# Kernel tuning notes

Measured on AMD Instinct MI355X. Metric: run time of the kernel, lower is better.

The kernel has to match this reference:

```python
import jax, jax.numpy as jnp
import numpy as np

NUM_DOTS = 100
IMG_SIZE = 4096


def setup_inputs() -> dict:
    key = jax.random.key(0)
    k1, k2, k3, k4 = jax.random.split(key, 4)
    adv_patch = jax.random.uniform(k1, (3, IMG_SIZE, IMG_SIZE), dtype=jnp.float32)
    centers = jax.random.uniform(k2, (NUM_DOTS, 2), dtype=jnp.float32)
    radii = jax.random.uniform(k3, (NUM_DOTS,), dtype=jnp.float32)
    colors = jax.random.uniform(k4, (NUM_DOTS, 3), dtype=jnp.float32)
    return {"adv_patch": adv_patch, "centers": centers, "radii": radii, "colors": colors}


def reference(adv_patch, centers, radii, colors):
    # Replicates PatchTrainer.forward: for each dot, draw a filled circle
    # (PIL ellipse with center (int(cx*S), int(cy*S)) and radius int(r*S/5))
    # and overwrite the three channels with the dot's color inside the circle.
    # Later dots overwrite earlier ones (sequential masked_fill_), so we scan.
    S = adv_patch.shape[-1]
    # int() truncation on non-negative values == floor
    xc = jnp.floor(centers[:, 0] * S)          # [N] horizontal center (image x)
    yc = jnp.floor(centers[:, 1] * S)          # [N] vertical center (image y)
    r = jnp.floor(radii * (S / 5.0))           # [N]
    xs = jnp.arange(S, dtype=adv_patch.dtype)  # columns (x)
    ys = jnp.arange(S, dtype=adv_patch.dtype)  # rows (y)

    def step(patch, dot):
        xci, yci, ri, col = dot
        # circle mask [S, S] indexed [y, x], matching ToTensor() layout
        d2 = (xs[None, :] - xci) ** 2 + (ys[:, None] - yci) ** 2
        mask = d2 <= ri * ri
        patch = jnp.where(mask[None, :, :], col[:, None, None], patch)
        return patch, None

    out, _ = jax.lax.scan(step, adv_patch, (xc, yc, r, colors))
    return out
```

## Files before the change

kernel.cpp:

```cpp
#include <hip/hip_runtime.h>


#define IMG  4096
#define ND   100
#define TW   256
#define TH   32
#define NBX  (IMG / TW)
#define NBY  (IMG / TH)

typedef float vfloat4 __attribute__((ext_vector_type(4)));

__global__ __launch_bounds__(256) void patch_dots_kernel(
    const float* __restrict__ patch,
    const float* __restrict__ centers,
    const float* __restrict__ radii,
    const float* __restrict__ colors,
    float* __restrict__ out)
{
    __shared__ float4 s_dot[ND];
    __shared__ unsigned long long s_mask[2];
    __shared__ int s_cnt;

    const int bid = blockIdx.x;
    const int bx  = bid % NBX;
    const int by  = (bid / NBX) % NBY;
    const int z   = bid / (NBX * NBY);

    const int tx0 = bx * TW;
    const int ty0 = by * TH;
    const int t   = threadIdx.x;
    const int lane = t & 63;
    const int w    = t >> 6;

    const size_t plane = (size_t)z * IMG * IMG;

    int flag = 0;
    float xc = 0.f, yc = 0.f, r2 = 0.f, col = 0.f;
    if (t < ND) {
        xc = floorf(centers[2 * t]     * 4096.0f);
        yc = floorf(centers[2 * t + 1] * 4096.0f);
        float r = floorf(radii[t] * (4096.0f / 5.0f));
        r2 = r * r;
        col = colors[3 * t + z];
        float cx = fminf(fmaxf(xc, (float)tx0), (float)(tx0 + TW - 1));
        float cy = fminf(fmaxf(yc, (float)ty0), (float)(ty0 + TH - 1));
        float dx = xc - cx, dy = yc - cy;
        flag = (dx * dx + dy * dy <= r2) ? 1 : 0;
    }
    if (t < 128) {
        unsigned long long m = __ballot(flag != 0);
        if (lane == 0) s_mask[w] = m;
    }
    __syncthreads();
    {
        const unsigned long long m0 = s_mask[0];
        if (flag) {
            const unsigned long long mw = s_mask[w];
            int pos = __popcll(mw & ((1ull << lane) - 1)) + (w ? __popcll(m0) : 0);
            s_dot[pos] = make_float4(xc, yc, r2, col);
        }
        if (t == 0) s_cnt = __popcll(m0) + __popcll(s_mask[1]);
    }
    __syncthreads();
    const int cnt = s_cnt;

    const int x0   = tx0 + lane * 4;
    const float fx0 = (float)x0;
    const float fx1 = (float)(x0 + 1);
    const float fx2 = (float)(x0 + 2);
    const float fx3 = (float)(x0 + 3);
    const float fxL = (float)tx0;
    const float fxR = (float)(tx0 + TW - 1);

    for (int it = 0; it < TH / 4; ++it) {
        const int   y  = ty0 + it * 4 + w;
        const float fy = (float)y;

        int b0 = -1, b1 = -1, b2 = -1, b3 = -1;
        for (int k = cnt - 1; k >= 0; --k) {
            const float4 d  = s_dot[k];
            const float dy  = fy - d.y;
            const float t2  = d.z - dy * dy;
            const float dl  = fxL - d.x;
            const float dr  = fxR - d.x;
            const bool  eL  = (dl * dl <= t2);
            const bool  eR  = (dr * dr <= t2);
            if (eL && eR) {
                if (b0 < 0) b0 = k;
                if (b1 < 0) b1 = k;
                if (b2 < 0) b2 = k;
                if (b3 < 0) b3 = k;
                break;
            }
            if (!eL && !eR && !(t2 >= 0.f && d.x >= fxL && d.x <= fxR)) continue;
            const float dx0 = fx0 - d.x;
            const float dx1 = fx1 - d.x;
            const float dx2 = fx2 - d.x;
            const float dx3 = fx3 - d.x;
            if (b0 < 0 && dx0 * dx0 <= t2) b0 = k;
            if (b1 < 0 && dx1 * dx1 <= t2) b1 = k;
            if (b2 < 0 && dx2 * dx2 <= t2) b2 = k;
            if (b3 < 0 && dx3 * dx3 <= t2) b3 = k;
            if (__all((b0 | b1 | b2 | b3) >= 0)) break;
        }

        const size_t base = plane + (size_t)y * IMG + x0;

        float4 p = make_float4(0.f, 0.f, 0.f, 0.f);
        if ((b0 | b1 | b2 | b3) < 0) {
            const vfloat4 pv = __builtin_nontemporal_load((const vfloat4*)(patch + base));
            p = make_float4(pv.x, pv.y, pv.z, pv.w);
        }

        vfloat4 o;
        o.x = (b0 >= 0) ? s_dot[b0].w : p.x;
        o.y = (b1 >= 0) ? s_dot[b1].w : p.y;
        o.z = (b2 >= 0) ? s_dot[b2].w : p.z;
        o.w = (b3 >= 0) ? s_dot[b3].w : p.w;

        __builtin_nontemporal_store(o, (vfloat4*)(out + base));
    }
}

extern "C" void kernel_launch(void* const* d_in, const int* in_sizes, int n_in,
                              void* d_out, int out_size, void* d_ws, size_t ws_size,
                              hipStream_t stream) {
    const float* patch   = (const float*)d_in[0];
    const float* centers = (const float*)d_in[1];
    const float* radii   = (const float*)d_in[2];
    const float* colors  = (const float*)d_in[3];
    float* out = (float*)d_out;

    dim3 grid(NBX * NBY * 3);
    dim3 block(256);
    patch_dots_kernel<<<grid, block, 0, stream>>>(patch, centers, radii, colors, out);
}
```

Before: 304.5 us.

## Precompute dot table in prep kernel and batch row stores per wave

Adds a small prep kernel that computes the floored center, squared radius and per-channel color for every dot into workspace, so each tile block loads one float4 per dot instead of recomputing from three scattered arrays. The main loop now gives each wave 8 consecutive rows instead of interleaved rows, unrolls them, keeps the results in registers and issues all stores at the end. The aim is to cut the per-block prologue cost and to improve memory-level parallelism on the streaming writes. In exchange it adds a second kernel launch and raises register pressure from the unrolled output buffer.

```diff
diff --git a/kernel.cpp b/kernel.cpp
--- a/kernel.cpp
+++ b/kernel.cpp
@@ -10,11 +10,28 @@
 
 typedef float vfloat4 __attribute__((ext_vector_type(4)));
 
-__global__ __launch_bounds__(256) void patch_dots_kernel(
-    const float* __restrict__ patch,
+__global__ __launch_bounds__(128) void prep_dots(
     const float* __restrict__ centers,
     const float* __restrict__ radii,
     const float* __restrict__ colors,
+    float4* __restrict__ table)
+{
+    const int i = threadIdx.x;
+    const int z = blockIdx.x;
+    if (i < ND) {
+        float xc = floorf(centers[2 * i]     * 4096.0f);
+        float yc = floorf(centers[2 * i + 1] * 4096.0f);
+        float r  = floorf(radii[i] * (4096.0f / 5.0f));
+        table[z * ND + i] = make_float4(xc, yc, r * r, colors[3 * i + z]);
+    }
+}
+
+__global__ __launch_bounds__(256) void patch_dots_kernel(
+    const float*  __restrict__ patch,
+    const float4* __restrict__ table,
+    const float*  __restrict__ centers,
+    const float*  __restrict__ radii,
+    const float*  __restrict__ colors,
     float* __restrict__ out)
 {
     __shared__ float4 s_dot[ND];
@@ -35,17 +52,20 @@
     const size_t plane = (size_t)z * IMG * IMG;
 
     int flag = 0;
-    float xc = 0.f, yc = 0.f, r2 = 0.f, col = 0.f;
+    float4 d4 = make_float4(0.f, 0.f, 0.f, 0.f);
     if (t < ND) {
-        xc = floorf(centers[2 * t]     * 4096.0f);
-        yc = floorf(centers[2 * t + 1] * 4096.0f);
-        float r = floorf(radii[t] * (4096.0f / 5.0f));
-        r2 = r * r;
-        col = colors[3 * t + z];
-        float cx = fminf(fmaxf(xc, (float)tx0), (float)(tx0 + TW - 1));
-        float cy = fminf(fmaxf(yc, (float)ty0), (float)(ty0 + TH - 1));
-        float dx = xc - cx, dy = yc - cy;
-        flag = (dx * dx + dy * dy <= r2) ? 1 : 0;
+        if (table) {
+            d4 = table[z * ND + t];
+        } else {
+            float xc = floorf(centers[2 * t]     * 4096.0f);
+            float yc = floorf(centers[2 * t + 1] * 4096.0f);
+            float r  = floorf(radii[t] * (4096.0f / 5.0f));
+            d4 = make_float4(xc, yc, r * r, colors[3 * t + z]);
+        }
+        float cx = fminf(fmaxf(d4.x, (float)tx0), (float)(tx0 + TW - 1));
+        float cy = fminf(fmaxf(d4.y, (float)ty0), (float)(ty0 + TH - 1));
+        float dx = d4.x - cx, dy = d4.y - cy;
+        flag = (dx * dx + dy * dy <= d4.z) ? 1 : 0;
     }
     if (t < 128) {
         unsigned long long m = __ballot(flag != 0);
@@ -57,7 +77,7 @@
         if (flag) {
             const unsigned long long mw = s_mask[w];
             int pos = __popcll(mw & ((1ull << lane) - 1)) + (w ? __popcll(m0) : 0);
-            s_dot[pos] = make_float4(xc, yc, r2, col);
+            s_dot[pos] = d4;
         }
         if (t == 0) s_cnt = __popcll(m0) + __popcll(s_mask[1]);
     }
@@ -72,9 +92,12 @@
     const float fxL = (float)tx0;
     const float fxR = (float)(tx0 + TW - 1);
 
-    for (int it = 0; it < TH / 4; ++it) {
-        const int   y  = ty0 + it * 4 + w;
-        const float fy = (float)y;
+    const int yb = ty0 + w * 8;
+    vfloat4 ov[8];
+
+    #pragma unroll
+    for (int it = 0; it < 8; ++it) {
+        const float fy = (float)(yb + it);
 
         int b0 = -1, b1 = -1, b2 = -1, b3 = -1;
         for (int k = cnt - 1; k >= 0; --k) {
@@ -104,22 +127,23 @@
             if (__all((b0 | b1 | b2 | b3) >= 0)) break;
         }
 
-        const size_t base = plane + (size_t)y * IMG + x0;
-
         float4 p = make_float4(0.f, 0.f, 0.f, 0.f);
         if ((b0 | b1 | b2 | b3) < 0) {
+            const size_t base = plane + (size_t)(yb + it) * IMG + x0;
             const vfloat4 pv = __builtin_nontemporal_load((const vfloat4*)(patch + base));
             p = make_float4(pv.x, pv.y, pv.z, pv.w);
         }
 
-        vfloat4 o;
-        o.x = (b0 >= 0) ? s_dot[b0].w : p.x;
-        o.y = (b1 >= 0) ? s_dot[b1].w : p.y;
-        o.z = (b2 >= 0) ? s_dot[b2].w : p.z;
-        o.w = (b3 >= 0) ? s_dot[b3].w : p.w;
+        ov[it].x = (b0 >= 0) ? s_dot[b0].w : p.x;
+        ov[it].y = (b1 >= 0) ? s_dot[b1].w : p.y;
+        ov[it].z = (b2 >= 0) ? s_dot[b2].w : p.z;
+        ov[it].w = (b3 >= 0) ? s_dot[b3].w : p.w;
+    }
 
-        __builtin_nontemporal_store(o, (vfloat4*)(out + base));
-    }
+    const size_t base0 = plane + (size_t)yb * IMG + x0;
+    #pragma unroll
+    for (int it = 0; it < 8; ++it)
+        __builtin_nontemporal_store(ov[it], (vfloat4*)(out + base0 + (size_t)it * IMG));
 }
 
 extern "C" void kernel_launch(void* const* d_in, const int* in_sizes, int n_in,
@@ -131,7 +155,14 @@
     const float* colors  = (const float*)d_in[3];
     float* out = (float*)d_out;
 
+    float4* table = nullptr;
+    if (d_ws && ws_size >= 3 * ND * sizeof(float4)) {
+        table = (float4*)d_ws;
+        prep_dots<<<dim3(3), dim3(128), 0, stream>>>(centers, radii, colors, table);
+    }
+
     dim3 grid(NBX * NBY * 3);
     dim3 block(256);
-    patch_dots_kernel<<<grid, block, 0, stream>>>(patch, centers, radii, colors, out);
+    patch_dots_kernel<<<grid, block, 0, stream>>>(patch, table, centers, radii,
+                                                  colors, out);
 }
```

Measured after the change: 306.5 us. No clear change (+0.7%).
